# Performance work log

Hardware: AMD Instinct MI355X
Metric: run time of the kernel (lower is better)

## Reference

```python
import jax, jax.numpy as jnp
import numpy as np
import math

N_HEAD = 16
HEAD_DIM = 64
BASE = 10000.0

def setup_inputs() -> dict:
    key = jax.random.key(0)
    k1, k2, k3, k4 = jax.random.split(key, 4)
    B, T, C = 2, 2048, 1024
    x = jax.random.normal(k1, (B, T, C), dtype=jnp.float32)
    w_attn = jax.random.normal(k2, (3 * C, C), dtype=jnp.float32) * 0.02
    w_proj = jax.random.normal(k3, (C, C), dtype=jnp.float32) * 0.02
    delta = jax.random.normal(k4, (N_HEAD, HEAD_DIM), dtype=jnp.float32) * 0.5
    return {"x": x, "w_attn": w_attn, "w_proj": w_proj, "delta": delta}

def reference(x, w_attn, w_proj, delta):
    B, T, C = x.shape
    H, D = N_HEAD, HEAD_DIM
    # qkv projection (nn.Linear, no bias): x @ W^T
    qkv = jnp.einsum('btc,ec->bte', x, w_attn)
    q, k, v = jnp.split(qkv, 3, axis=-1)
    q = q.reshape(B, T, H, D).transpose(0, 2, 1, 3)  # (B,H,T,D)
    k = k.reshape(B, T, H, D).transpose(0, 2, 1, 3)
    v = v.reshape(B, T, H, D).transpose(0, 2, 1, 3)
    # PoPE: d frequencies per head
    inv_freq = 1.0 / (BASE ** (jnp.arange(D, dtype=jnp.float32) / D))  # (D,)
    t = jnp.arange(T, dtype=jnp.float32)
    freqs = t[:, None] * inv_freq[None, :]            # (T,D)
    cos_pos = jnp.cos(freqs)[None, None]              # (1,1,T,D)
    sin_pos = jnp.sin(freqs)[None, None]
    mu_q = jax.nn.softplus(q)
    mu_k = jax.nn.softplus(k)
    d = jnp.clip(delta, -2.0 * math.pi, 0.0)          # (H,D)
    cos_d = jnp.cos(d)[None, :, None, :]              # (1,H,1,D)
    sin_d = jnp.sin(d)[None, :, None, :]
    q_real = mu_q * cos_pos
    q_imag = mu_q * sin_pos
    k_real = mu_k * (cos_pos * cos_d - sin_pos * sin_d)
    k_imag = mu_k * (sin_pos * cos_d + cos_pos * sin_d)
    scale = 1.0 / math.sqrt(D)
    att = (jnp.einsum('bhtd,bhsd->bhts', q_real, k_real)
           + jnp.einsum('bhtd,bhsd->bhts', q_imag, k_imag)) * scale
    causal = jnp.tril(jnp.ones((T, T), dtype=bool))
    att = jnp.where(causal[None, None], att, -jnp.inf)
    att = jax.nn.softmax(att, axis=-1)
    y = jnp.einsum('bhts,bhsd->bhtd', att, v)
    y = y.transpose(0, 2, 1, 3).reshape(B, T, C)
    return jnp.einsum('btc,ec->bte', y, w_proj)
```

## Files before the change

### kernel.cpp

```cpp
#include <hip/hip_runtime.h>
#include <math.h>

typedef short s16x8 __attribute__((ext_vector_type(8)));
typedef float f32x4 __attribute__((ext_vector_type(4)));
typedef float f32x16 __attribute__((ext_vector_type(16)));
typedef unsigned short u16;

#define B_ 2
#define T_ 2048
#define HN_ 16

__device__ __forceinline__ u16 f2bf(float f) {
  union { float f; unsigned u; } v; v.f = f;
  unsigned r = v.u + 0x7FFFu + ((v.u >> 16) & 1u);
  return (u16)(r >> 16);
}
__device__ __forceinline__ float bf2f(u16 b) {
  union { unsigned u; float f; } v; v.u = ((unsigned)b) << 16;
  return v.f;
}
__device__ __forceinline__ float softplus_f(float v) {
  return fmaxf(v, 0.f) + __logf(1.f + __expf(-fabsf(v)));
}
__device__ __forceinline__ f32x4 mfma16(s16x8 a, s16x8 b, f32x4 c) {
  return __builtin_amdgcn_mfma_f32_16x16x32_bf16(a, b, c, 0, 0, 0);
}
__device__ __forceinline__ f32x16 mfma32(s16x8 a, s16x8 b, f32x16 c) {
  return __builtin_amdgcn_mfma_f32_32x32x16_bf16(a, b, c, 0, 0, 0);
}
__device__ __forceinline__ void gload16(void* lds, const void* g) {
  __builtin_amdgcn_global_load_lds(
      (const __attribute__((address_space(1))) unsigned int*)g,
      (__attribute__((address_space(3))) unsigned int*)lds, 16, 0, 0);
}
__device__ __forceinline__ unsigned cvtpk(float lo, float hi) {
  unsigned r;
  asm("v_cvt_pk_bf16_f32 %0, %1, %2" : "=v"(r) : "v"(lo), "v"(hi));
  return r;
}

__device__ __constant__ unsigned char QTC[72][3] = {
  {15,0,64},{15,1,65},{15,2,66},{15,3,67},{15,4,68},{15,5,69},{15,6,70},{15,7,71},
  {14,0,56},{14,1,57},{14,2,58},{14,3,59},{14,4,60},{14,5,61},{14,6,62},{14,7,63},
  {13,0,49},{13,1,50},{13,2,51},{13,3,52},{13,4,53},{13,5,54},{13,6,55},
  {12,0,42},{12,1,43},{12,2,44},{12,3,45},{12,4,46},{12,5,47},{12,6,48},
  {11,0,36},{11,1,37},{11,2,38},{11,3,39},{11,4,40},{11,5,41},
  {10,0,30},{10,1,31},{10,2,32},{10,3,33},{10,4,34},{10,5,35},
  {9,0,25},{9,1,26},{9,2,27},{9,3,28},{9,4,29},
  {8,0,20},{8,1,21},{8,2,22},{8,3,23},{8,4,24},
  {7,0,16},{7,1,17},{7,2,18},{7,3,19},
  {6,0,12},{6,1,13},{6,2,14},{6,3,15},
  {5,0,9},{5,1,10},{5,2,11},
  {4,0,6},{4,1,7},{4,2,8},
  {3,0,4},{3,1,5},
  {2,0,2},{2,1,3},
  {1,0,1},
  {0,0,0}
};
__device__ __constant__ unsigned char OFFT[16] =
  {0,1,2,4,6,9,12,16,20,25,30,36,42,49,56,64};

__global__ __launch_bounds__(256) void conv_swz(
    const float* __restrict__ in, u16* __restrict__ out, int nchunks)
{
  int c = blockIdx.x * 256 + threadIdx.x;
  if (c >= nchunks) return;
  int row = c >> 7, cc = c & 127;
  int ks = cc >> 3, ch = cc & 7;
  const float4* src = (const float4*)(in + ((size_t)row << 10) + (cc << 3));
  float4 a = src[0], b = src[1];
  s16x8 o;
  o[0] = (short)f2bf(a.x); o[1] = (short)f2bf(a.y);
  o[2] = (short)f2bf(a.z); o[3] = (short)f2bf(a.w);
  o[4] = (short)f2bf(b.x); o[5] = (short)f2bf(b.y);
  o[6] = (short)f2bf(b.z); o[7] = (short)f2bf(b.w);
  *(s16x8*)(out + ((size_t)row << 10) + (ks << 6) + ((ch ^ (row & 7)) << 3)) = o;
}

__global__ __launch_bounds__(256) void build_tables(
    float* __restrict__ postab, float* __restrict__ dtab,
    const float* __restrict__ delta)
{
  int idx = blockIdx.x * 256 + threadIdx.x;
  int t = idx >> 6, d = idx & 63;
  float invf = powf(10000.f, -(float)d * (1.0f / 64.0f));
  float ang = (float)t * invf;
  float sp, cp;
  sincosf(ang, &sp, &cp);
  postab[idx * 2 + 0] = cp;
  postab[idx * 2 + 1] = sp;
  if (idx < HN_ * 64) {
    float dl = delta[idx];
    dl = fminf(fmaxf(dl, -6.2831853071795865f), 0.f);
    float sd, cd;
    sincosf(dl, &sd, &cd);
    dtab[idx * 2 + 0] = cd;
    dtab[idx * 2 + 1] = sd;
  }
}

template<int OUTK>
__global__ __launch_bounds__(256) void gemm_nt_mfma(
    const u16* __restrict__ A, const u16* __restrict__ Bw,
    void* __restrict__ Cout, int N)
{
  __shared__ u16 As[128 * 64];
  __shared__ u16 Bs[128 * 64];
  const int tid = threadIdx.x;
  const int w = tid >> 6, l = tid & 63, g = l >> 4;
  const int bm = blockIdx.y * 128, bn = blockIdx.x * 128;
  const int wr = w >> 1, wc = w & 1;
  const int K = 1024;

  const f32x4 zero = {0.f, 0.f, 0.f, 0.f};
  f32x4 acc[4][4];
  #pragma unroll
  for (int mt = 0; mt < 4; ++mt)
    #pragma unroll
    for (int nt = 0; nt < 4; ++nt) acc[mt][nt] = zero;

  for (int kt = 0; kt < K; kt += 64) {
    __syncthreads();
    #pragma unroll
    for (int j = 0; j < 4; ++j) {
      int cid = (j * 4 + w) * 64 + l;
      int row = cid >> 3, cc = cid & 7;
      gload16(As + ((j * 4 + w) << 9), A  + (size_t)(bm + row) * K + kt + cc * 8);
      gload16(Bs + ((j * 4 + w) << 9), Bw + (size_t)(bn + row) * K + kt + cc * 8);
    }
    __syncthreads();
    #pragma unroll
    for (int ks = 0; ks < 2; ++ks) {
      s16x8 af[4], bfr[4];
      #pragma unroll
      for (int mt = 0; mt < 4; ++mt) {
        int rr = wr * 64 + mt * 16 + (l & 15);
        af[mt] = *(const s16x8*)(As + rr * 64 + (((ks * 4 + g) ^ (rr & 7)) << 3));
      }
      #pragma unroll
      for (int nt = 0; nt < 4; ++nt) {
        int rr = wc * 64 + nt * 16 + (l & 15);
        bfr[nt] = *(const s16x8*)(Bs + rr * 64 + (((ks * 4 + g) ^ (rr & 7)) << 3));
      }
      #pragma unroll
      for (int mt = 0; mt < 4; ++mt)
        #pragma unroll
        for (int nt = 0; nt < 4; ++nt)
          acc[mt][nt] = mfma16(af[mt], bfr[nt], acc[mt][nt]);
    }
  }

  #pragma unroll
  for (int mt = 0; mt < 4; ++mt)
    #pragma unroll
    for (int nt = 0; nt < 4; ++nt)
      #pragma unroll
      for (int r = 0; r < 4; ++r) {
        int row = bm + wr * 64 + mt * 16 + g * 4 + r;
        int col = bn + wc * 64 + nt * 16 + (l & 15);
        if (OUTK == 0)
          ((u16*)Cout)[(size_t)row * N + col] = f2bf(acc[mt][nt][r]);
        else
          ((float*)Cout)[(size_t)row * N + col] = acc[mt][nt][r];
      }
}

__global__ __launch_bounds__(256) void pope_prep(
    const u16* __restrict__ qkvb, const float* __restrict__ postab,
    const float* __restrict__ dtab, u16* __restrict__ Kp, u16* __restrict__ Vtp,
    u16* __restrict__ Qp, float* __restrict__ qn, int* __restrict__ knmaxI)
{
  __shared__ u16 Vs[64][72];
  __shared__ float knsh[64];
  const int tb = blockIdx.x, h = blockIdx.y, b = blockIdx.z;
  const int t0 = tb * 64, tid = threadIdx.x;
  const int tl = tid >> 2, j = tid & 3, d0 = j * 16;
  const int t = t0 + tl;
  const size_t bh = (size_t)b * HN_ + h;
  const size_t qrow = (size_t)(b * T_ + t) * 3072 + h * 64;
  const float2* pt = (const float2*)postab + (size_t)t * 64 + d0;

  float kss = 0.f;
  {
    s16x8 k0 = *(const s16x8*)(qkvb + qrow + 1024 + d0);
    s16x8 k1 = *(const s16x8*)(qkvb + qrow + 1024 + d0 + 8);
    const float2* dt = (const float2*)dtab + h * 64 + d0;
    s16x8 r0, r1, i0, i1;
    #pragma unroll
    for (int i = 0; i < 8; ++i) {
      float mu = softplus_f(bf2f((u16)k0[i]));
      kss += mu * mu;
      float2 cs = pt[i]; float2 dc = dt[i];
      r0[i] = (short)f2bf(mu * (cs.x * dc.x - cs.y * dc.y));
      i0[i] = (short)f2bf(mu * (cs.y * dc.x + cs.x * dc.y));
    }
    #pragma unroll
    for (int i = 0; i < 8; ++i) {
      float mu = softplus_f(bf2f((u16)k1[i]));
      kss += mu * mu;
      float2 cs = pt[8 + i]; float2 dc = dt[8 + i];
      r1[i] = (short)f2bf(mu * (cs.x * dc.x - cs.y * dc.y));
      i1[i] = (short)f2bf(mu * (cs.y * dc.x + cs.x * dc.y));
    }
    u16* Krow = Kp + (bh * T_ + t) * 128;
    int sw = t & 7;
    int c0 = d0 >> 3;
    *(s16x8*)(Krow + ((c0 ^ sw) << 3))       = r0;
    *(s16x8*)(Krow + (((c0 + 1) ^ sw) << 3)) = r1;
    *(s16x8*)(Krow + (((c0 + 8) ^ sw) << 3)) = i0;
    *(s16x8*)(Krow + (((c0 + 9) ^ sw) << 3)) = i1;
  }
  kss += __shfl_xor(kss, 1);
  kss += __shfl_xor(kss, 2);
  if (j == 0) knsh[tl] = kss;

  float qss = 0.f;
  {
    s16x8 q0 = *(const s16x8*)(qkvb + qrow + d0);
    s16x8 q1 = *(const s16x8*)(qkvb + qrow + d0 + 8);
    s16x8 r0, r1, i0, i1;
    #pragma unroll
    for (int i = 0; i < 8; ++i) {
      float mu = softplus_f(bf2f((u16)q0[i]));
      qss += mu * mu;
      float2 cs = pt[i];
      r0[i] = (short)f2bf(mu * cs.x);
      i0[i] = (short)f2bf(mu * cs.y);
    }
    #pragma unroll
    for (int i = 0; i < 8; ++i) {
      float mu = softplus_f(bf2f((u16)q1[i]));
      qss += mu * mu;
      float2 cs = pt[8 + i];
      r1[i] = (short)f2bf(mu * cs.x);
      i1[i] = (short)f2bf(mu * cs.y);
    }
    u16* Qrow = Qp + (bh * T_ + t) * 128;
    *(s16x8*)(Qrow + d0)          = r0;
    *(s16x8*)(Qrow + d0 + 8)      = r1;
    *(s16x8*)(Qrow + 64 + d0)     = i0;
    *(s16x8*)(Qrow + 64 + d0 + 8) = i1;
  }
  qss += __shfl_xor(qss, 1);
  qss += __shfl_xor(qss, 2);
  if (j == 0) qn[bh * T_ + t] = sqrtf(qss);

  {
    s16x8 v0 = *(const s16x8*)(qkvb + qrow + 2048 + d0);
    s16x8 v1 = *(const s16x8*)(qkvb + qrow + 2048 + d0 + 8);
    *(s16x8*)(&Vs[tl][d0])     = v0;
    *(s16x8*)(&Vs[tl][d0 + 8]) = v1;
  }
  __syncthreads();
  if (tid == 0) {
    float mx = 0.f;
    #pragma unroll
    for (int i = 0; i < 64; ++i) mx = fmaxf(mx, knsh[i]);
    atomicMax(knmaxI + bh, __float_as_int(sqrtf(mx)));
  }
  {
    const int d = tid >> 2, jj = tid & 3, ts0 = jj * 16;
    u16* Vrow = Vtp + (bh * 64 + d) * T_;
    int swd = d & 7;
    s16x8 o0, o1;
    #pragma unroll
    for (int i = 0; i < 8; ++i) {
      o0[i] = (short)Vs[ts0 + i][d];
      o1[i] = (short)Vs[ts0 + 8 + i][d];
    }
    int cc0 = ts0 >> 3;
    *(s16x8*)(Vrow + t0 + ((cc0 ^ swd) << 3))       = o0;
    *(s16x8*)(Vrow + t0 + (((cc0 + 1) ^ swd) << 3)) = o1;
  }
}

__global__ __launch_bounds__(256) void attn_split(
    const u16* __restrict__ Qp, const u16* __restrict__ Kp,
    const u16* __restrict__ Vtp, const float* __restrict__ qn,
    const int* __restrict__ knmaxI, u16* __restrict__ po, float* __restrict__ pl)
{
  const int xcd = (int)blockIdx.x & 7;
  const int idx = (int)blockIdx.x >> 3;
  const int bh = xcd + 8 * (idx / 72);
  const int w72 = idx % 72;
  const int qt = QTC[w72][0], c = QTC[w72][1];
  const int slot = bh * 72 + QTC[w72][2];

  __shared__ u16 smem[2][12288];
  const int tid = threadIdx.x, w = tid >> 6, l = tid & 63;
  const int hi = l >> 5, ln = l & 31;

  const int kbeg = c * 256;
  const int kend0 = (qt + 1) * 128;
  const int kend = kend0 < kbeg + 256 ? kend0 : kbeg + 256;
  const int ntile = (kend - kbeg) >> 6;

  const float LS = 0.125f * 1.4426950408889634f;
  const u16* Kpb = Kp + (size_t)bh * T_ * 128;
  const u16* Vtb = Vtp + (size_t)bh * 64 * T_;

  auto STAGE = [&](int buf, int s0) {
    u16* Kd = smem[buf];
    u16* Vd = smem[buf] + 8192;
    #pragma unroll
    for (int jj = 0; jj < 4; ++jj) {
      int cid = (jj * 4 + w) * 64 + l;
      int row = cid >> 4, cc = cid & 15;
      gload16(Kd + ((jj * 4 + w) << 9), Kpb + (size_t)(s0 + row) * 128 + cc * 8);
    }
    #pragma unroll
    for (int jj = 0; jj < 2; ++jj) {
      int cid = (jj * 4 + w) * 64 + l;
      int row = cid >> 3, cc = cid & 7;
      gload16(Vd + ((jj * 4 + w) << 9), Vtb + (size_t)row * T_ + s0 + cc * 8);
    }
  };

  STAGE(0, kbeg);

  const int q = qt * 128 + w * 32 + ln;
  s16x8 qf[8];
  {
    const u16* qrp = Qp + ((size_t)bh * T_ + q) * 128;
    #pragma unroll
    for (int ks = 0; ks < 8; ++ks)
      qf[ks] = *(const s16x8*)(qrp + ks * 16 + hi * 8);
  }
  const float knm = __int_as_float(knmaxI[bh]);
  const float m = LS * qn[(size_t)bh * T_ + q] * knm;

  STAGE(1, kbeg + 64);

  const f32x16 zero16 = {0.f,0.f,0.f,0.f,0.f,0.f,0.f,0.f,
                         0.f,0.f,0.f,0.f,0.f,0.f,0.f,0.f};
  f32x16 o0 = zero16, o1 = zero16;
  float lsum = 0.f;
  const int qminw = qt * 128 + w * 32;

  for (int ti = 0; ti < ntile; ++ti) {
    const int s0 = kbeg + ti * 64;
    if (ti + 1 < ntile)
      asm volatile("s_waitcnt vmcnt(6)" ::: "memory");
    else
      asm volatile("s_waitcnt vmcnt(0)" ::: "memory");
    __builtin_amdgcn_s_barrier();
    __builtin_amdgcn_sched_barrier(0);

    const u16* Ks  = smem[ti & 1];
    const u16* Vts = smem[ti & 1] + 8192;

    if (s0 <= qminw + 31) {
      const bool needmask = (s0 + 63) > qminw;

      f32x16 sacc0 = zero16, sacc1 = zero16;
      __builtin_amdgcn_s_setprio(1);
      #pragma unroll
      for (int ks = 0; ks < 8; ++ks) {
        int r0_ = ln, r1_ = 32 + ln;
        s16x8 kf0 = *(const s16x8*)(Ks + r0_ * 128 + (((2 * ks + hi) ^ (r0_ & 7)) << 3));
        s16x8 kf1 = *(const s16x8*)(Ks + r1_ * 128 + (((2 * ks + hi) ^ (r1_ & 7)) << 3));
        sacc0 = mfma32(kf0, qf[ks], sacc0);
        sacc1 = mfma32(kf1, qf[ks], sacc1);
      }
      __builtin_amdgcn_s_setprio(0);

      if (needmask) {
        #pragma unroll
        for (int jj = 0; jj < 16; ++jj) {
          int sg = s0 + (jj & 3) + 8 * (jj >> 2) + 4 * hi;
          if (sg > q)      sacc0[jj] = -3e38f;
          if (sg + 32 > q) sacc1[jj] = -3e38f;
        }
      }
      float rs = 0.f;
      #pragma unroll
      for (int jj = 0; jj < 16; ++jj) {
        float p0 = exp2f(fmaf(sacc0[jj], LS, -m));
        float p1 = exp2f(fmaf(sacc1[jj], LS, -m));
        sacc0[jj] = p0; sacc1[jj] = p1;
        rs += p0 + p1;
      }
      lsum += rs;

      s16x8 pa[4];
      #pragma unroll
      for (int ks = 0; ks < 4; ++ks) {
        const int bb = (ks & 1) * 8;
        unsigned a0, a1, b0v, b1v;
        if (ks < 2) {
          a0  = cvtpk(sacc0[bb + 0], sacc0[bb + 1]);
          a1  = cvtpk(sacc0[bb + 2], sacc0[bb + 3]);
          b0v = cvtpk(sacc0[bb + 4], sacc0[bb + 5]);
          b1v = cvtpk(sacc0[bb + 6], sacc0[bb + 7]);
        } else {
          a0  = cvtpk(sacc1[bb + 0], sacc1[bb + 1]);
          a1  = cvtpk(sacc1[bb + 2], sacc1[bb + 3]);
          b0v = cvtpk(sacc1[bb + 4], sacc1[bb + 5]);
          b1v = cvtpk(sacc1[bb + 6], sacc1[bb + 7]);
        }
        asm("v_permlane32_swap_b32 %0, %1" : "+v"(a0), "+v"(b0v));
        asm("v_permlane32_swap_b32 %0, %1" : "+v"(a1), "+v"(b1v));
        union { unsigned u[4]; s16x8 v; } pu;
        pu.u[0] = a0; pu.u[1] = a1; pu.u[2] = b0v; pu.u[3] = b1v;
        pa[ks] = pu.v;
      }

      __builtin_amdgcn_s_setprio(1);
      #pragma unroll
      for (int ks = 0; ks < 4; ++ks) {
        int rd0 = ln, rd1 = 32 + ln;
        s16x8 vb0 = *(const s16x8*)(Vts + rd0 * 64 + (((2 * ks + hi) ^ (rd0 & 7)) << 3));
        s16x8 vb1 = *(const s16x8*)(Vts + rd1 * 64 + (((2 * ks + hi) ^ (rd1 & 7)) << 3));
        o0 = mfma32(pa[ks], vb0, o0);
        o1 = mfma32(pa[ks], vb1, o1);
      }
      __builtin_amdgcn_s_setprio(0);
    }
    __builtin_amdgcn_s_barrier();
    if (ti + 2 < ntile) STAGE(ti & 1, s0 + 128);
  }

  lsum += __shfl_xor(lsum, 32);
  u16* pob = po + (size_t)slot * 8192;
  #pragma unroll
  for (int jj = 0; jj < 16; ++jj) {
    int row = w * 32 + 4 * hi + (jj & 3) + 8 * (jj >> 2);
    pob[row * 64 + ln]      = f2bf(o0[jj]);
    pob[row * 64 + 32 + ln] = f2bf(o1[jj]);
  }
  if (hi == 0)
    pl[(size_t)slot * 128 + w * 32 + ln] = lsum;
}

__global__ __launch_bounds__(256) void attn_combine(
    const u16* __restrict__ po, const float* __restrict__ pl,
    u16* __restrict__ yb)
{
  const int xcd = (int)blockIdx.x & 7;
  const int i = (int)blockIdx.x >> 3;
  const int bh = xcd + 8 * (i & 3);
  const int qt = 15 - (i >> 2);
  const int b = bh >> 4, h = bh & 15;
  const int nch = (qt + 2) >> 1;
  const int base = bh * 72 + OFFT[qt];
  const int t = threadIdx.x;
  const int row = t >> 1, d0 = (t & 1) * 32;

  float acc[32];
  #pragma unroll
  for (int i2 = 0; i2 < 32; ++i2) acc[i2] = 0.f;
  float ls = 0.f;
  for (int c = 0; c < nch; ++c) {
    const u16* pr = po + (size_t)(base + c) * 8192 + row * 64 + d0;
    #pragma unroll
    for (int v = 0; v < 4; ++v) {
      s16x8 x = *(const s16x8*)(pr + v * 8);
      #pragma unroll
      for (int i2 = 0; i2 < 8; ++i2) acc[v * 8 + i2] += bf2f((u16)x[i2]);
    }
    ls += pl[(size_t)(base + c) * 128 + row];
  }
  float inv = 1.f / ls;
  int qrow = qt * 128 + row;
  size_t rb = (size_t)(b * T_ + qrow) * 1024 + h * 64;
  #pragma unroll
  for (int v = 0; v < 4; ++v) {
    int ch = ((d0 >> 3) + v) ^ (qrow & 7);
    s16x8 o;
    #pragma unroll
    for (int i2 = 0; i2 < 8; ++i2) o[i2] = (short)f2bf(acc[v * 8 + i2] * inv);
    *(s16x8*)(yb + rb + (ch << 3)) = o;
  }
}

extern "C" void kernel_launch(void* const* d_in, const int* in_sizes, int n_in,
                              void* d_out, int out_size, void* d_ws, size_t ws_size,
                              hipStream_t stream)
{
  const float* x      = (const float*)d_in[0];
  const float* w_attn = (const float*)d_in[1];
  const float* w_proj = (const float*)d_in[2];
  const float* delta  = (const float*)d_in[3];
  float* out = (float*)d_out;

  char* p = (char*)d_ws;
  u16* qkvb   = (u16*)p;
  u16* xb     = (u16*)(p + (size_t)4096 * 3072 * 2);
  u16* wab    = (u16*)(p + (size_t)4096 * 3072 * 2 + (size_t)4096 * 1024 * 2);
  u16* po     = (u16*)p;
  p += (size_t)(4096 * 3072 + 4096 * 1024 + 3072 * 1024) * 2;
  u16* wpb    = (u16*)p;  p += (size_t)1024 * 1024 * 2;
  u16* yb     = (u16*)p;  p += (size_t)4096 * 1024 * 2;
  u16* Kp     = (u16*)p;  p += (size_t)B_ * HN_ * T_ * 128 * 2;
  u16* Vtp    = (u16*)p;  p += (size_t)B_ * HN_ * 64 * T_ * 2;
  u16* Qp     = (u16*)p;  p += (size_t)B_ * HN_ * T_ * 128 * 2;
  float* postab = (float*)p; p += (size_t)T_ * 64 * 2 * 4;
  float* dtab   = (float*)p; p += (size_t)HN_ * 64 * 2 * 4;
  float* qn     = (float*)p; p += (size_t)B_ * HN_ * T_ * 4;
  float* pl     = (float*)p; p += (size_t)2304 * 128 * 4;
  int*   knmaxI = (int*)p;   p += 32 * 4;

  conv_swz<<<(4096 * 128) / 256, 256, 0, stream>>>(x, xb, 4096 * 128);
  conv_swz<<<(3072 * 128) / 256, 256, 0, stream>>>(w_attn, wab, 3072 * 128);
  conv_swz<<<(1024 * 128) / 256, 256, 0, stream>>>(w_proj, wpb, 1024 * 128);
  build_tables<<<(T_ * 64) / 256, 256, 0, stream>>>(postab, dtab, delta);
  hipMemsetAsync(knmaxI, 0, 32 * 4, stream);

  gemm_nt_mfma<0><<<dim3(3072 / 128, 4096 / 128), 256, 0, stream>>>(xb, wab, qkvb, 3072);
  pope_prep<<<dim3(T_ / 64, HN_, B_), 256, 0, stream>>>(qkvb, postab, dtab, Kp, Vtp,
                                                        Qp, qn, knmaxI);
  attn_split<<<dim3(2304), 256, 0, stream>>>(Qp, Kp, Vtp, qn, knmaxI, po, pl);
  attn_combine<<<dim3(512), 256, 0, stream>>>(po, pl, yb);
  gemm_nt_mfma<1><<<dim3(1024 / 128, 4096 / 128), 256, 0, stream>>>(yb, wpb, out, 1024);
}
```

Measured before the change: 162.6 us.

## Fuse prep kernels into one launch and widen QKV GEMM tile to 128x256

The three fp32-to-bf16 swizzle conversions, the sin/cos table build and the memset are merged into a single prep_all kernel, replacing five stream operations with one launch. The QKV projection GEMM moves to a new 512-thread kernel with a 128x256 output tile, so each A tile loaded from global memory is reused across twice as many output columns. The larger block uses more LDS and launches fewer blocks (384 instead of 768), which may change occupancy and tail behaviour.

```diff
diff --git a/kernel.cpp b/kernel.cpp
--- a/kernel.cpp
+++ b/kernel.cpp
@@ -60,11 +60,9 @@
 __device__ __constant__ unsigned char OFFT[16] =
   {0,1,2,4,6,9,12,16,20,25,30,36,42,49,56,64};
 
-__global__ __launch_bounds__(256) void conv_swz(
-    const float* __restrict__ in, u16* __restrict__ out, int nchunks)
-{
-  int c = blockIdx.x * 256 + threadIdx.x;
-  if (c >= nchunks) return;
+__device__ __forceinline__ void conv_one(
+    const float* __restrict__ in, u16* __restrict__ out, int c)
+{
   int row = c >> 7, cc = c & 127;
   int ks = cc >> 3, ch = cc & 7;
   const float4* src = (const float4*)(in + ((size_t)row << 10) + (cc << 3));
@@ -77,25 +75,37 @@
   *(s16x8*)(out + ((size_t)row << 10) + (ks << 6) + ((ch ^ (row & 7)) << 3)) = o;
 }
 
-__global__ __launch_bounds__(256) void build_tables(
-    float* __restrict__ postab, float* __restrict__ dtab,
-    const float* __restrict__ delta)
-{
-  int idx = blockIdx.x * 256 + threadIdx.x;
-  int t = idx >> 6, d = idx & 63;
-  float invf = powf(10000.f, -(float)d * (1.0f / 64.0f));
-  float ang = (float)t * invf;
-  float sp, cp;
-  sincosf(ang, &sp, &cp);
-  postab[idx * 2 + 0] = cp;
-  postab[idx * 2 + 1] = sp;
-  if (idx < HN_ * 64) {
-    float dl = delta[idx];
-    dl = fminf(fmaxf(dl, -6.2831853071795865f), 0.f);
-    float sd, cd;
-    sincosf(dl, &sd, &cd);
-    dtab[idx * 2 + 0] = cd;
-    dtab[idx * 2 + 1] = sd;
+__global__ __launch_bounds__(256) void prep_all(
+    const float* __restrict__ x, const float* __restrict__ w_attn,
+    const float* __restrict__ w_proj, const float* __restrict__ delta,
+    u16* __restrict__ xb, u16* __restrict__ wab, u16* __restrict__ wpb,
+    float* __restrict__ postab, float* __restrict__ dtab, int* __restrict__ knmaxI)
+{
+  const int gid = blockIdx.x * 256 + threadIdx.x;
+  if (gid < 32) knmaxI[gid] = 0;
+  if (gid < 524288) {
+    conv_one(x, xb, gid);
+  } else if (gid < 917504) {
+    conv_one(w_attn, wab, gid - 524288);
+  } else if (gid < 1048576) {
+    conv_one(w_proj, wpb, gid - 917504);
+  } else {
+    int idx = gid - 1048576;
+    int t = idx >> 6, d = idx & 63;
+    float invf = powf(10000.f, -(float)d * (1.0f / 64.0f));
+    float ang = (float)t * invf;
+    float sp, cp;
+    sincosf(ang, &sp, &cp);
+    postab[idx * 2 + 0] = cp;
+    postab[idx * 2 + 1] = sp;
+    if (idx < HN_ * 64) {
+      float dl = delta[idx];
+      dl = fminf(fmaxf(dl, -6.2831853071795865f), 0.f);
+      float sd, cd;
+      sincosf(dl, &sd, &cd);
+      dtab[idx * 2 + 0] = cd;
+      dtab[idx * 2 + 1] = sd;
+    }
   }
 }
 
@@ -162,6 +172,75 @@
           ((u16*)Cout)[(size_t)row * N + col] = f2bf(acc[mt][nt][r]);
         else
           ((float*)Cout)[(size_t)row * N + col] = acc[mt][nt][r];
+      }
+}
+
+__global__ __launch_bounds__(512) void gemm_nt_mfma256(
+    const u16* __restrict__ A, const u16* __restrict__ Bw,
+    u16* __restrict__ Cout, int N)
+{
+  __shared__ u16 As[128 * 64];
+  __shared__ u16 Bs[256 * 64];
+  const int tid = threadIdx.x;
+  const int w = tid >> 6, l = tid & 63, g = l >> 4;
+  const int bm = blockIdx.y * 128, bn = blockIdx.x * 256;
+  const int wr = w >> 2, wc = w & 3;
+  const int K = 1024;
+
+  const f32x4 zero = {0.f, 0.f, 0.f, 0.f};
+  f32x4 acc[4][4];
+  #pragma unroll
+  for (int mt = 0; mt < 4; ++mt)
+    #pragma unroll
+    for (int nt = 0; nt < 4; ++nt) acc[mt][nt] = zero;
+
+  for (int kt = 0; kt < K; kt += 64) {
+    __syncthreads();
+    #pragma unroll
+    for (int j = 0; j < 2; ++j) {
+      int grp = j * 8 + w;
+      int cid = grp * 64 + l;
+      int row = cid >> 3, cc = cid & 7;
+      gload16(As + (grp << 9), A + (size_t)(bm + row) * K + kt + cc * 8);
+    }
+    #pragma unroll
+    for (int j = 0; j < 4; ++j) {
+      int grp = j * 8 + w;
+      int cid = grp * 64 + l;
+      int row = cid >> 3, cc = cid & 7;
+      gload16(Bs + (grp << 9), Bw + (size_t)(bn + row) * K + kt + cc * 8);
+    }
+    __syncthreads();
+    #pragma unroll
+    for (int ks = 0; ks < 2; ++ks) {
+      s16x8 af[4], bfr[4];
+      #pragma unroll
+      for (int mt = 0; mt < 4; ++mt) {
+        int rr = wr * 64 + mt * 16 + (l & 15);
+        af[mt] = *(const s16x8*)(As + rr * 64 + (((ks * 4 + g) ^ (rr & 7)) << 3));
+      }
+      #pragma unroll
+      for (int nt = 0; nt < 4; ++nt) {
+        int rr = wc * 64 + nt * 16 + (l & 15);
+        bfr[nt] = *(const s16x8*)(Bs + rr * 64 + (((ks * 4 + g) ^ (rr & 7)) << 3));
+      }
+      #pragma unroll
+      for (int mt = 0; mt < 4; ++mt)
+        #pragma unroll
+        for (int nt = 0; nt < 4; ++nt)
+          acc[mt][nt] = mfma16(af[mt], bfr[nt], acc[mt][nt]);
+    }
+  }
+
+  #pragma unroll
+  for (int mt = 0; mt < 4; ++mt)
+    #pragma unroll
+    for (int nt = 0; nt < 4; ++nt)
+      #pragma unroll
+      for (int r = 0; r < 4; ++r) {
+        int row = bm + wr * 64 + mt * 16 + g * 4 + r;
+        int col = bn + wc * 64 + nt * 16 + (l & 15);
+        Cout[(size_t)row * N + col] = f2bf(acc[mt][nt][r]);
       }
 }
 
@@ -500,13 +579,11 @@
   float* pl     = (float*)p; p += (size_t)2304 * 128 * 4;
   int*   knmaxI = (int*)p;   p += 32 * 4;
 
-  conv_swz<<<(4096 * 128) / 256, 256, 0, stream>>>(x, xb, 4096 * 128);
-  conv_swz<<<(3072 * 128) / 256, 256, 0, stream>>>(w_attn, wab, 3072 * 128);
-  conv_swz<<<(1024 * 128) / 256, 256, 0, stream>>>(w_proj, wpb, 1024 * 128);
-  build_tables<<<(T_ * 64) / 256, 256, 0, stream>>>(postab, dtab, delta);
-  hipMemsetAsync(knmaxI, 0, 32 * 4, stream);
-
-  gemm_nt_mfma<0><<<dim3(3072 / 128, 4096 / 128), 256, 0, stream>>>(xb, wab, qkvb, 3072);
+  prep_all<<<dim3((1048576 + T_ * 64) / 256), 256, 0, stream>>>(
+      x, w_attn, w_proj, delta, xb, wab, wpb, postab, dtab, knmaxI);
+
+  gemm_nt_mfma256<<<dim3(3072 / 256, 4096 / 128), 512, 0, stream>>>(
+      xb, wab, qkvb, 3072);
   pope_prep<<<dim3(T_ / 64, HN_, B_), 256, 0, stream>>>(qkvb, postab, dtab, Kp, Vtp,
                                                         Qp, qn, knmaxI);
   attn_split<<<dim3(2304), 256, 0, stream>>>(Qp, Kp, Vtp, qn, knmaxI, po, pl);
```

After: 171.8 us. +5.6%, slower.
